# Kernel tuning notes

Measured on AMD Instinct MI355X. Metric: run time of the kernel, lower is better.

## Reference

```python
import jax, jax.numpy as jnp
import numpy as np

EPS = 1e-4  # clamp from module default (0.0001, 1 - 0.0001)


def setup_inputs() -> dict:
    key = jax.random.key(0)
    k1, k2, k3 = jax.random.split(key, 3)
    B, T, C, K = 16, 4096, 512, 3
    x = jax.random.normal(k1, (B, T, C), dtype=jnp.float32)
    # logit_alpha initialized as logit of (0.8, 0.9, 0.98) tiled across channels
    init_alphas = jnp.array([0.8, 0.9, 0.98], dtype=jnp.float32)
    logit_alpha = jnp.broadcast_to(
        (jnp.log(init_alphas) - jnp.log1p(-init_alphas))[:, None], (K, C)
    ).astype(jnp.float32)
    # add small noise so gradients are non-degenerate
    logit_alpha = logit_alpha + 0.01 * jax.random.normal(k2, (K, C), dtype=jnp.float32)
    mix_logits = 0.1 * jax.random.normal(k3, (C, K), dtype=jnp.float32)
    return {"x": x, "logit_alpha": logit_alpha, "mix_logits": mix_logits}


def reference(x, logit_alpha, mix_logits):
    # x: [B,T,C]; logit_alpha: [K,C]; mix_logits: [C,K]
    B, T, C = x.shape
    K = logit_alpha.shape[0]
    a = jnp.clip(jax.nn.sigmoid(logit_alpha), EPS, 1.0 - EPS)  # [K,C]
    b = 1.0 - a

    y0 = jnp.broadcast_to(x[:, 0, None, :], (B, K, C))  # t=0: y = x0 for all K

    def step(y_prev, xt):
        # y_prev: [B,K,C], xt: [B,C]
        y = a * y_prev + b * xt[:, None, :]
        return y, y

    xs = jnp.swapaxes(x[:, 1:, :], 0, 1)  # [T-1,B,C]
    _, ys = jax.lax.scan(step, y0, xs)  # [T-1,B,K,C]
    yk = jnp.concatenate([y0[None], ys], axis=0)  # [T,B,K,C]

    mix = jax.nn.softmax(mix_logits, axis=-1)  # [C,K]
    trend = jnp.einsum('tbkc,ck->tbc', yk, mix)  # [T,B,C]
    return jnp.swapaxes(trend, 0, 1)  # [B,T,C]
```

## Files before the change

kernel.cpp:

```cpp
#include <hip/hip_runtime.h>

#define DEV_INLINE __device__ __forceinline__

constexpr int B = 16, T = 4096, C = 512, K = 3;
constexpr int NC = 64;
constexpr int L  = T / NC;
constexpr int C4 = C / 4;
constexpr float EPS = 1e-4f;

constexpr size_t TAB_A     = 0;
constexpr size_t TAB_AL    = (size_t)K * C;
constexpr size_t TAB_MIX   = (size_t)2 * K * C;
constexpr size_t CARRY_OFF = (size_t)4 * K * C;

DEV_INLINE float4 f4mul(float4 a, float4 b) {
  return make_float4(a.x * b.x, a.y * b.y, a.z * b.z, a.w * b.w);
}
DEV_INLINE float4 f4fma(float4 a, float4 b, float4 c) {
  return make_float4(fmaf(a.x, b.x, c.x), fmaf(a.y, b.y, c.y),
                     fmaf(a.z, b.z, c.z), fmaf(a.w, b.w, c.w));
}
DEV_INLINE float4 f4onesub(float4 a) {
  return make_float4(1.f - a.x, 1.f - a.y, 1.f - a.z, 1.f - a.w);
}

__global__ void ema_prep(const float* __restrict__ logit_alpha,
                         const float* __restrict__ mix_logits,
                         float* __restrict__ ws) {
  int c = blockIdx.x * blockDim.x + threadIdx.x;
  if (c >= C) return;
  #pragma unroll
  for (int k = 0; k < K; ++k) {
    float la = logit_alpha[k * C + c];
    float a  = 1.0f / (1.0f + __expf(-la));
    a = fminf(fmaxf(a, EPS), 1.0f - EPS);
    ws[TAB_A + k * C + c] = a;
    float p = a;
    #pragma unroll
    for (int s = 0; s < 6; ++s) p = p * p;
    ws[TAB_AL + k * C + c] = p;
  }
  float m0 = mix_logits[c * K + 0];
  float m1 = mix_logits[c * K + 1];
  float m2 = mix_logits[c * K + 2];
  float mx = fmaxf(m0, fmaxf(m1, m2));
  float e0 = __expf(m0 - mx), e1 = __expf(m1 - mx), e2 = __expf(m2 - mx);
  float inv = 1.0f / (e0 + e1 + e2);
  ws[TAB_MIX + 0 * C + c] = e0 * inv;
  ws[TAB_MIX + 1 * C + c] = e1 * inv;
  ws[TAB_MIX + 2 * C + c] = e2 * inv;
}

__global__ __launch_bounds__(128) void ema_pass1(const float* __restrict__ x,
                                                 float* __restrict__ ws) {
  const int c4 = threadIdx.x;
  const int bi = blockIdx.x;
  const int i  = bi & (NC - 1);

  const float4* aT = (const float4*)(ws + TAB_A);
  const float4 a0 = aT[0 * C4 + c4];
  const float4 a1 = aT[1 * C4 + c4];
  const float4 a2 = aT[2 * C4 + c4];
  const float4 b0 = f4onesub(a0), b1 = f4onesub(a1), b2 = f4onesub(a2);

  const float4* xb = (const float4*)x + (size_t)bi * L * C4 + c4;

  float4 y0, y1, y2;
  int jstart;
  if (i == 0) {
    float4 x0 = xb[0];
    y0 = x0; y1 = x0; y2 = x0;
    jstart = 1;
  } else {
    y0 = make_float4(0.f, 0.f, 0.f, 0.f);
    y1 = y0; y2 = y0;
    jstart = 0;
  }

  #pragma unroll 4
  for (int j = jstart; j < L; ++j) {
    float4 xv = xb[(size_t)j * C4];
    y0 = f4fma(a0, y0, f4mul(b0, xv));
    y1 = f4fma(a1, y1, f4mul(b1, xv));
    y2 = f4fma(a2, y2, f4mul(b2, xv));
  }

  float4* carry = (float4*)(ws + CARRY_OFF);
  const size_t cb = ((size_t)bi * K) * C4 + c4;
  carry[cb + 0 * C4] = y0;
  carry[cb + 1 * C4] = y1;
  carry[cb + 2 * C4] = y2;
}

__global__ __launch_bounds__(256) void ema_pass2(float* __restrict__ ws) {
  int idx = blockIdx.x * blockDim.x + threadIdx.x;
  if (idx >= B * K * C4) return;
  const int c4 = idx % C4;
  const int k  = (idx / C4) % K;
  const int b  = idx / (C4 * K);

  const float4 A = ((const float4*)(ws + TAB_AL))[k * C4 + c4];
  float4* carry = (float4*)(ws + CARRY_OFF);
  const size_t stride = (size_t)K * C4;
  const size_t base = ((size_t)b * NC) * stride + (size_t)k * C4 + c4;

  float4 S = carry[base];
  for (int i = 1; i < NC; ++i) {
    const size_t idxi = base + (size_t)i * stride;
    float4 t = carry[idxi];
    carry[idxi] = S;
    S = f4fma(A, S, t);
  }
}

__global__ __launch_bounds__(128) void ema_pass3(const float* __restrict__ x,
                                                 const float* __restrict__ ws,
                                                 float* __restrict__ out) {
  const int c4 = threadIdx.x;
  const int bi = blockIdx.x;
  const int i  = bi & (NC - 1);

  const float4* aT = (const float4*)(ws + TAB_A);
  const float4* mT = (const float4*)(ws + TAB_MIX);
  const float4 a0 = aT[0 * C4 + c4];
  const float4 a1 = aT[1 * C4 + c4];
  const float4 a2 = aT[2 * C4 + c4];
  const float4 b0 = f4onesub(a0), b1 = f4onesub(a1), b2 = f4onesub(a2);
  const float4 m0 = mT[0 * C4 + c4];
  const float4 m1 = mT[1 * C4 + c4];
  const float4 m2 = mT[2 * C4 + c4];

  const float4* xb = (const float4*)x   + (size_t)bi * L * C4 + c4;
  float4*       ob = (float4*)out       + (size_t)bi * L * C4 + c4;
  const float4* carry = (const float4*)(ws + CARRY_OFF);

  float4 y0, y1, y2;
  int jstart;
  if (i == 0) {
    float4 x0 = xb[0];
    y0 = x0; y1 = x0; y2 = x0;
    ob[0] = f4fma(m0, y0, f4fma(m1, y1, f4mul(m2, y2)));
    jstart = 1;
  } else {
    const size_t cb = ((size_t)bi * K) * C4 + c4;
    y0 = carry[cb + 0 * C4];
    y1 = carry[cb + 1 * C4];
    y2 = carry[cb + 2 * C4];
    jstart = 0;
  }

  #pragma unroll 4
  for (int j = jstart; j < L; ++j) {
    float4 xv = xb[(size_t)j * C4];
    y0 = f4fma(a0, y0, f4mul(b0, xv));
    y1 = f4fma(a1, y1, f4mul(b1, xv));
    y2 = f4fma(a2, y2, f4mul(b2, xv));
    ob[(size_t)j * C4] = f4fma(m0, y0, f4fma(m1, y1, f4mul(m2, y2)));
  }
}

extern "C" void kernel_launch(void* const* d_in, const int* in_sizes, int n_in,
                              void* d_out, int out_size, void* d_ws, size_t ws_size,
                              hipStream_t stream) {
  const float* x           = (const float*)d_in[0];
  const float* logit_alpha = (const float*)d_in[1];
  const float* mix_logits  = (const float*)d_in[2];
  float* out = (float*)d_out;
  float* ws  = (float*)d_ws;

  ema_prep<<<(C + 255) / 256, 256, 0, stream>>>(logit_alpha, mix_logits, ws);
  ema_pass1<<<B * NC, 128, 0, stream>>>(x, ws);
  ema_pass2<<<(B * K * C4 + 255) / 256, 256, 0, stream>>>(ws);
  ema_pass3<<<B * NC, 128, 0, stream>>>(x, ws, out);
}
```

Before: 268.6 us.

## Split scan into more chunks with hierarchical two-level carry propagation

Raises the chunk count from 64 to 256 per batch, so pass1 and pass3 each launch 4096 blocks, and replaces the serial 64-step carry scan with two levels. The first level scans groups of 16 chunks and the second scans the group totals using a^(16L). Pass3 rebuilds each chunk's true carry from the local and group carries, with the power of a_L computed by binary exponentiation. The goal is more parallelism and a shorter serial dependency chain in the carry scan. The cost is an extra kernel launch, more carry traffic, and occupancy hints added through launch bounds.

```diff
diff --git a/kernel.cpp b/kernel.cpp
--- a/kernel.cpp
+++ b/kernel.cpp
@@ -3,15 +3,19 @@
 #define DEV_INLINE __device__ __forceinline__
 
 constexpr int B = 16, T = 4096, C = 512, K = 3;
-constexpr int NC = 64;
+constexpr int NC = 256;
 constexpr int L  = T / NC;
 constexpr int C4 = C / 4;
+constexpr int GS = 16;
+constexpr int G  = NC / GS;
 constexpr float EPS = 1e-4f;
 
-constexpr size_t TAB_A     = 0;
-constexpr size_t TAB_AL    = (size_t)K * C;
-constexpr size_t TAB_MIX   = (size_t)2 * K * C;
-constexpr size_t CARRY_OFF = (size_t)4 * K * C;
+constexpr size_t TAB_A   = 0;
+constexpr size_t TAB_AL  = (size_t)1 * K * C;
+constexpr size_t TAB_A16 = (size_t)2 * K * C;
+constexpr size_t TAB_MIX = (size_t)3 * K * C;
+constexpr size_t CARRY   = (size_t)4 * K * C;
+constexpr size_t GCARRY  = CARRY + (size_t)B * NC * K * C;
 
 DEV_INLINE float4 f4mul(float4 a, float4 b) {
   return make_float4(a.x * b.x, a.y * b.y, a.z * b.z, a.w * b.w);
@@ -20,9 +24,14 @@
   return make_float4(fmaf(a.x, b.x, c.x), fmaf(a.y, b.y, c.y),
                      fmaf(a.z, b.z, c.z), fmaf(a.w, b.w, c.w));
 }
+DEV_INLINE float4 f4add(float4 a, float4 b) {
+  return make_float4(a.x + b.x, a.y + b.y, a.z + b.z, a.w + b.w);
+}
 DEV_INLINE float4 f4onesub(float4 a) {
   return make_float4(1.f - a.x, 1.f - a.y, 1.f - a.z, 1.f - a.w);
 }
+DEV_INLINE float4 f4zero() { return make_float4(0.f, 0.f, 0.f, 0.f); }
+DEV_INLINE float4 f4one()  { return make_float4(1.f, 1.f, 1.f, 1.f); }
 
 __global__ void ema_prep(const float* __restrict__ logit_alpha,
                          const float* __restrict__ mix_logits,
@@ -37,8 +46,11 @@
     ws[TAB_A + k * C + c] = a;
     float p = a;
     #pragma unroll
-    for (int s = 0; s < 6; ++s) p = p * p;
+    for (int s = 0; s < 4; ++s) p = p * p;
     ws[TAB_AL + k * C + c] = p;
+    #pragma unroll
+    for (int s = 0; s < 4; ++s) p = p * p;
+    ws[TAB_A16 + k * C + c] = p;
   }
   float m0 = mix_logits[c * K + 0];
   float m1 = mix_logits[c * K + 1];
@@ -51,8 +63,8 @@
   ws[TAB_MIX + 2 * C + c] = e2 * inv;
 }
 
-__global__ __launch_bounds__(128) void ema_pass1(const float* __restrict__ x,
-                                                 float* __restrict__ ws) {
+__global__ __launch_bounds__(128, 8) void ema_pass1(const float* __restrict__ x,
+                                                    float* __restrict__ ws) {
   const int c4 = threadIdx.x;
   const int bi = blockIdx.x;
   const int i  = bi & (NC - 1);
@@ -72,8 +84,7 @@
     y0 = x0; y1 = x0; y2 = x0;
     jstart = 1;
   } else {
-    y0 = make_float4(0.f, 0.f, 0.f, 0.f);
-    y1 = y0; y2 = y0;
+    y0 = f4zero(); y1 = y0; y2 = y0;
     jstart = 0;
   }
 
@@ -85,40 +96,69 @@
     y2 = f4fma(a2, y2, f4mul(b2, xv));
   }
 
-  float4* carry = (float4*)(ws + CARRY_OFF);
+  float4* carry = (float4*)(ws + CARRY);
   const size_t cb = ((size_t)bi * K) * C4 + c4;
   carry[cb + 0 * C4] = y0;
   carry[cb + 1 * C4] = y1;
   carry[cb + 2 * C4] = y2;
 }
 
-__global__ __launch_bounds__(256) void ema_pass2(float* __restrict__ ws) {
+__global__ __launch_bounds__(256) void ema_pass2a(float* __restrict__ ws) {
   int idx = blockIdx.x * blockDim.x + threadIdx.x;
-  if (idx >= B * K * C4) return;
-  const int c4 = idx % C4;
-  const int k  = (idx / C4) % K;
+  const int c4 = idx & (C4 - 1);
+  int r = idx >> 7;
+  const int k = r % K; r /= K;
+  const int g = r & (G - 1);
+  const int b = r >> 4;
+
+  const float4 A = ((const float4*)(ws + TAB_AL))[k * C4 + c4];
+  float4* carry = (float4*)(ws + CARRY);
+  float4* gcarry = (float4*)(ws + GCARRY);
+
+  const size_t cstride = (size_t)K * C4;
+  size_t slot = ((size_t)(b * NC + g * GS) * K + k) * (size_t)C4 + c4;
+
+  float4 P = f4zero();
+  #pragma unroll 4
+  for (int j = 0; j < GS; ++j) {
+    float4 t = carry[slot];
+    carry[slot] = P;
+    P = f4fma(A, P, t);
+    slot += cstride;
+  }
+  gcarry[((size_t)(b * G + g) * K + k) * C4 + c4] = P;
+}
+
+__global__ __launch_bounds__(256) void ema_pass2b(float* __restrict__ ws) {
+  int idx = blockIdx.x * blockDim.x + threadIdx.x;
+  const int c4 = idx & (C4 - 1);
+  const int k  = (idx >> 7) % K;
   const int b  = idx / (C4 * K);
 
-  const float4 A = ((const float4*)(ws + TAB_AL))[k * C4 + c4];
-  float4* carry = (float4*)(ws + CARRY_OFF);
-  const size_t stride = (size_t)K * C4;
-  const size_t base = ((size_t)b * NC) * stride + (size_t)k * C4 + c4;
-
-  float4 S = carry[base];
-  for (int i = 1; i < NC; ++i) {
-    const size_t idxi = base + (size_t)i * stride;
-    float4 t = carry[idxi];
-    carry[idxi] = S;
-    S = f4fma(A, S, t);
-  }
-}
-
-__global__ __launch_bounds__(128) void ema_pass3(const float* __restrict__ x,
-                                                 const float* __restrict__ ws,
-                                                 float* __restrict__ out) {
+  const float4 A16 = ((const float4*)(ws + TAB_A16))[k * C4 + c4];
+  float4* gcarry = (float4*)(ws + GCARRY);
+  const size_t gstride = (size_t)K * C4;
+  size_t slot = ((size_t)(b * G) * K + k) * (size_t)C4 + c4;
+
+  float4 S = f4zero();
+  #pragma unroll 4
+  for (int g = 0; g < G; ++g) {
+    float4 t = gcarry[slot];
+    gcarry[slot] = S;
+    S = f4fma(A16, S, t);
+    slot += gstride;
+  }
+}
+
+__global__ __launch_bounds__(128, 6) void ema_pass3(const float* __restrict__ x,
+                                                    const float* __restrict__ ws,
+                                                    float* __restrict__ out) {
   const int c4 = threadIdx.x;
   const int bi = blockIdx.x;
   const int i  = bi & (NC - 1);
+  const int b  = bi >> 8;
+  const int g  = i >> 4;
+  const int jl = i & (GS - 1);
 
   const float4* aT = (const float4*)(ws + TAB_A);
   const float4* mT = (const float4*)(ws + TAB_MIX);
@@ -130,9 +170,8 @@
   const float4 m1 = mT[1 * C4 + c4];
   const float4 m2 = mT[2 * C4 + c4];
 
-  const float4* xb = (const float4*)x   + (size_t)bi * L * C4 + c4;
-  float4*       ob = (float4*)out       + (size_t)bi * L * C4 + c4;
-  const float4* carry = (const float4*)(ws + CARRY_OFF);
+  const float4* xb = (const float4*)x + (size_t)bi * L * C4 + c4;
+  float4*       ob = (float4*)out     + (size_t)bi * L * C4 + c4;
 
   float4 y0, y1, y2;
   int jstart;
@@ -142,10 +181,30 @@
     ob[0] = f4fma(m0, y0, f4fma(m1, y1, f4mul(m2, y2)));
     jstart = 1;
   } else {
+    const float4* carry  = (const float4*)(ws + CARRY);
+    const float4* gcarry = (const float4*)(ws + GCARRY);
+    const float4* alT    = (const float4*)(ws + TAB_AL);
+
     const size_t cb = ((size_t)bi * K) * C4 + c4;
-    y0 = carry[cb + 0 * C4];
-    y1 = carry[cb + 1 * C4];
-    y2 = carry[cb + 2 * C4];
+    float4 l0 = carry[cb + 0 * C4];
+    float4 l1 = carry[cb + 1 * C4];
+    float4 l2 = carry[cb + 2 * C4];
+    const size_t gb = ((size_t)(b * G + g) * K) * C4 + c4;
+    float4 s0 = gcarry[gb + 0 * C4];
+    float4 s1 = gcarry[gb + 1 * C4];
+    float4 s2 = gcarry[gb + 2 * C4];
+    float4 p0 = f4one(), p1 = f4one(), p2 = f4one();
+    float4 q0 = alT[0 * C4 + c4];
+    float4 q1 = alT[1 * C4 + c4];
+    float4 q2 = alT[2 * C4 + c4];
+    #pragma unroll
+    for (int bit = 0; bit < 4; ++bit) {
+      if ((jl >> bit) & 1) { p0 = f4mul(p0, q0); p1 = f4mul(p1, q1); p2 = f4mul(p2, q2); }
+      if (bit < 3) { q0 = f4mul(q0, q0); q1 = f4mul(q1, q1); q2 = f4mul(q2, q2); }
+    }
+    y0 = f4fma(p0, s0, l0);
+    y1 = f4fma(p1, s1, l1);
+    y2 = f4fma(p2, s2, l2);
     jstart = 0;
   }
 
@@ -170,6 +229,7 @@
 
   ema_prep<<<(C + 255) / 256, 256, 0, stream>>>(logit_alpha, mix_logits, ws);
   ema_pass1<<<B * NC, 128, 0, stream>>>(x, ws);
-  ema_pass2<<<(B * K * C4 + 255) / 256, 256, 0, stream>>>(ws);
+  ema_pass2a<<<(B * G * K * C4) / 256, 256, 0, stream>>>(ws);
+  ema_pass2b<<<(B * K * C4 + 255) / 256, 256, 0, stream>>>(ws);
   ema_pass3<<<B * NC, 128, 0, stream>>>(x, ws, out);
 }
```

After: 283.6 us. +5.6%, slower.

## Fuse prep and carry-scan into chunk kernels, double chunk count to 128

Applied to the files above, without the earlier changes.

Removes the separate parameter-prep and carry-propagation kernels: each chunk kernel recomputes sigmoid/softmax coefficients inline, and the final pass serially folds all preceding chunk carries itself using a^32. Chunk count goes from 64 to 128 per batch to raise parallelism. This cuts two launches and the serial pass-2 kernel, at the cost of redundant carry reads (up to 127 per block, quadratic total but small) and recomputed transcendentals per block.

```diff
diff --git a/kernel.cpp b/kernel.cpp
--- a/kernel.cpp
+++ b/kernel.cpp
@@ -3,15 +3,11 @@
 #define DEV_INLINE __device__ __forceinline__
 
 constexpr int B = 16, T = 4096, C = 512, K = 3;
-constexpr int NC = 64;
-constexpr int L  = T / NC;
-constexpr int C4 = C / 4;
+constexpr int G    = 128;
+constexpr int Lseg = T / G;
+constexpr int C4   = C / 4;
 constexpr float EPS = 1e-4f;
 
-constexpr size_t TAB_A     = 0;
-constexpr size_t TAB_AL    = (size_t)K * C;
-constexpr size_t TAB_MIX   = (size_t)2 * K * C;
-constexpr size_t CARRY_OFF = (size_t)4 * K * C;
 
 DEV_INLINE float4 f4mul(float4 a, float4 b) {
   return make_float4(a.x * b.x, a.y * b.y, a.z * b.z, a.w * b.w);
@@ -23,134 +19,125 @@
 DEV_INLINE float4 f4onesub(float4 a) {
   return make_float4(1.f - a.x, 1.f - a.y, 1.f - a.z, 1.f - a.w);
 }
+DEV_INLINE float4 f4zero() { return make_float4(0.f, 0.f, 0.f, 0.f); }
 
-__global__ void ema_prep(const float* __restrict__ logit_alpha,
-                         const float* __restrict__ mix_logits,
-                         float* __restrict__ ws) {
-  int c = blockIdx.x * blockDim.x + threadIdx.x;
-  if (c >= C) return;
-  #pragma unroll
-  for (int k = 0; k < K; ++k) {
-    float la = logit_alpha[k * C + c];
-    float a  = 1.0f / (1.0f + __expf(-la));
-    a = fminf(fmaxf(a, EPS), 1.0f - EPS);
-    ws[TAB_A + k * C + c] = a;
-    float p = a;
-    #pragma unroll
-    for (int s = 0; s < 6; ++s) p = p * p;
-    ws[TAB_AL + k * C + c] = p;
-  }
-  float m0 = mix_logits[c * K + 0];
-  float m1 = mix_logits[c * K + 1];
-  float m2 = mix_logits[c * K + 2];
-  float mx = fmaxf(m0, fmaxf(m1, m2));
-  float e0 = __expf(m0 - mx), e1 = __expf(m1 - mx), e2 = __expf(m2 - mx);
-  float inv = 1.0f / (e0 + e1 + e2);
-  ws[TAB_MIX + 0 * C + c] = e0 * inv;
-  ws[TAB_MIX + 1 * C + c] = e1 * inv;
-  ws[TAB_MIX + 2 * C + c] = e2 * inv;
+DEV_INLINE float sig_clamp(float la) {
+  float a = 1.0f / (1.0f + __expf(-la));
+  return fminf(fmaxf(a, EPS), 1.0f - EPS);
+}
+DEV_INLINE float4 sig4(float4 la) {
+  return make_float4(sig_clamp(la.x), sig_clamp(la.y), sig_clamp(la.z), sig_clamp(la.w));
 }
 
-__global__ __launch_bounds__(128) void ema_pass1(const float* __restrict__ x,
-                                                 float* __restrict__ ws) {
+__global__ __launch_bounds__(128) void ema_k1(const float* __restrict__ x,
+                                              const float* __restrict__ logit_alpha,
+                                              float* __restrict__ ws) {
   const int c4 = threadIdx.x;
   const int bi = blockIdx.x;
-  const int i  = bi & (NC - 1);
+  const int g  = bi & (G - 1);
 
-  const float4* aT = (const float4*)(ws + TAB_A);
-  const float4 a0 = aT[0 * C4 + c4];
-  const float4 a1 = aT[1 * C4 + c4];
-  const float4 a2 = aT[2 * C4 + c4];
+  const float4* laT = (const float4*)logit_alpha;
+  const float4 a0 = sig4(laT[0 * C4 + c4]);
+  const float4 a1 = sig4(laT[1 * C4 + c4]);
+  const float4 a2 = sig4(laT[2 * C4 + c4]);
   const float4 b0 = f4onesub(a0), b1 = f4onesub(a1), b2 = f4onesub(a2);
 
-  const float4* xb = (const float4*)x + (size_t)bi * L * C4 + c4;
+  const float4* xb = (const float4*)x + (size_t)bi * Lseg * C4 + c4;
 
   float4 y0, y1, y2;
   int jstart;
-  if (i == 0) {
+  if (g == 0) {
     float4 x0 = xb[0];
     y0 = x0; y1 = x0; y2 = x0;
     jstart = 1;
   } else {
-    y0 = make_float4(0.f, 0.f, 0.f, 0.f);
-    y1 = y0; y2 = y0;
+    y0 = f4zero(); y1 = y0; y2 = y0;
     jstart = 0;
   }
 
   #pragma unroll 4
-  for (int j = jstart; j < L; ++j) {
+  for (int j = jstart; j < Lseg; ++j) {
     float4 xv = xb[(size_t)j * C4];
     y0 = f4fma(a0, y0, f4mul(b0, xv));
     y1 = f4fma(a1, y1, f4mul(b1, xv));
     y2 = f4fma(a2, y2, f4mul(b2, xv));
   }
 
-  float4* carry = (float4*)(ws + CARRY_OFF);
-  const size_t cb = ((size_t)bi * K) * C4 + c4;
-  carry[cb + 0 * C4] = y0;
-  carry[cb + 1 * C4] = y1;
-  carry[cb + 2 * C4] = y2;
+  float4* gc = (float4*)ws;
+  const size_t cb = (size_t)bi * K * C4 + c4;
+  gc[cb + 0 * C4] = y0;
+  gc[cb + 1 * C4] = y1;
+  gc[cb + 2 * C4] = y2;
 }
 
-__global__ __launch_bounds__(256) void ema_pass2(float* __restrict__ ws) {
-  int idx = blockIdx.x * blockDim.x + threadIdx.x;
-  if (idx >= B * K * C4) return;
-  const int c4 = idx % C4;
-  const int k  = (idx / C4) % K;
-  const int b  = idx / (C4 * K);
-
-  const float4 A = ((const float4*)(ws + TAB_AL))[k * C4 + c4];
-  float4* carry = (float4*)(ws + CARRY_OFF);
-  const size_t stride = (size_t)K * C4;
-  const size_t base = ((size_t)b * NC) * stride + (size_t)k * C4 + c4;
-
-  float4 S = carry[base];
-  for (int i = 1; i < NC; ++i) {
-    const size_t idxi = base + (size_t)i * stride;
-    float4 t = carry[idxi];
-    carry[idxi] = S;
-    S = f4fma(A, S, t);
-  }
-}
-
-__global__ __launch_bounds__(128) void ema_pass3(const float* __restrict__ x,
-                                                 const float* __restrict__ ws,
-                                                 float* __restrict__ out) {
+__global__ __launch_bounds__(128) void ema_k2(const float* __restrict__ x,
+                                              const float* __restrict__ logit_alpha,
+                                              const float* __restrict__ mix_logits,
+                                              const float* __restrict__ ws,
+                                              float* __restrict__ out) {
   const int c4 = threadIdx.x;
   const int bi = blockIdx.x;
-  const int i  = bi & (NC - 1);
+  const int g  = bi & (G - 1);
+  const int b  = bi >> 7;
 
-  const float4* aT = (const float4*)(ws + TAB_A);
-  const float4* mT = (const float4*)(ws + TAB_MIX);
-  const float4 a0 = aT[0 * C4 + c4];
-  const float4 a1 = aT[1 * C4 + c4];
-  const float4 a2 = aT[2 * C4 + c4];
+  const float4* laT = (const float4*)logit_alpha;
+  const float4 a0 = sig4(laT[0 * C4 + c4]);
+  const float4 a1 = sig4(laT[1 * C4 + c4]);
+  const float4 a2 = sig4(laT[2 * C4 + c4]);
   const float4 b0 = f4onesub(a0), b1 = f4onesub(a1), b2 = f4onesub(a2);
-  const float4 m0 = mT[0 * C4 + c4];
-  const float4 m1 = mT[1 * C4 + c4];
-  const float4 m2 = mT[2 * C4 + c4];
 
-  const float4* xb = (const float4*)x   + (size_t)bi * L * C4 + c4;
-  float4*       ob = (float4*)out       + (size_t)bi * L * C4 + c4;
-  const float4* carry = (const float4*)(ws + CARRY_OFF);
+  float mm0[4], mm1[4], mm2[4];
+  #pragma unroll
+  for (int u = 0; u < 4; ++u) {
+    const int c = 4 * c4 + u;
+    float l0 = mix_logits[c * K + 0];
+    float l1 = mix_logits[c * K + 1];
+    float l2 = mix_logits[c * K + 2];
+    float mx = fmaxf(l0, fmaxf(l1, l2));
+    float e0 = __expf(l0 - mx), e1 = __expf(l1 - mx), e2 = __expf(l2 - mx);
+    float inv = 1.0f / (e0 + e1 + e2);
+    mm0[u] = e0 * inv; mm1[u] = e1 * inv; mm2[u] = e2 * inv;
+  }
+  const float4 m0 = make_float4(mm0[0], mm0[1], mm0[2], mm0[3]);
+  const float4 m1 = make_float4(mm1[0], mm1[1], mm1[2], mm1[3]);
+  const float4 m2 = make_float4(mm2[0], mm2[1], mm2[2], mm2[3]);
+
+  float4 A0 = a0, A1 = a1, A2 = a2;
+  #pragma unroll
+  for (int s = 0; s < 5; ++s) { A0 = f4mul(A0, A0); A1 = f4mul(A1, A1); A2 = f4mul(A2, A2); }
+
+  float4 S0 = f4zero(), S1 = S0, S2 = S0;
+  {
+    const float4* gc = (const float4*)ws;
+    size_t slot = ((size_t)b * G) * K * C4 + c4;
+    for (int gp = 0; gp < g; ++gp) {
+      float4 t0 = gc[slot + 0 * C4];
+      float4 t1 = gc[slot + 1 * C4];
+      float4 t2 = gc[slot + 2 * C4];
+      S0 = f4fma(A0, S0, t0);
+      S1 = f4fma(A1, S1, t1);
+      S2 = f4fma(A2, S2, t2);
+      slot += (size_t)K * C4;
+    }
+  }
+
+  const float4* xb = (const float4*)x + (size_t)bi * Lseg * C4 + c4;
+  float4*       ob = (float4*)out     + (size_t)bi * Lseg * C4 + c4;
 
   float4 y0, y1, y2;
   int jstart;
-  if (i == 0) {
+  if (g == 0) {
     float4 x0 = xb[0];
     y0 = x0; y1 = x0; y2 = x0;
     ob[0] = f4fma(m0, y0, f4fma(m1, y1, f4mul(m2, y2)));
     jstart = 1;
   } else {
-    const size_t cb = ((size_t)bi * K) * C4 + c4;
-    y0 = carry[cb + 0 * C4];
-    y1 = carry[cb + 1 * C4];
-    y2 = carry[cb + 2 * C4];
+    y0 = S0; y1 = S1; y2 = S2;
     jstart = 0;
   }
 
   #pragma unroll 4
-  for (int j = jstart; j < L; ++j) {
+  for (int j = jstart; j < Lseg; ++j) {
     float4 xv = xb[(size_t)j * C4];
     y0 = f4fma(a0, y0, f4mul(b0, xv));
     y1 = f4fma(a1, y1, f4mul(b1, xv));
@@ -168,8 +155,6 @@
   float* out = (float*)d_out;
   float* ws  = (float*)d_ws;
 
-  ema_prep<<<(C + 255) / 256, 256, 0, stream>>>(logit_alpha, mix_logits, ws);
-  ema_pass1<<<B * NC, 128, 0, stream>>>(x, ws);
-  ema_pass2<<<(B * K * C4 + 255) / 256, 256, 0, stream>>>(ws);
-  ema_pass3<<<B * NC, 128, 0, stream>>>(x, ws, out);
+  ema_k1<<<B * G, 128, 0, stream>>>(x, logit_alpha, ws);
+  ema_k2<<<B * G, 128, 0, stream>>>(x, logit_alpha, mix_logits, ws, out);
 }
```

Measured after the change: 313.4 us. 16.7% more time.
